# Kernel tuning notes

Hardware: AMD Instinct MI355X
Metric: run time of the kernel (lower is better)

Reference implementation:

```python
import jax, jax.numpy as jnp
import numpy as np

# ---- model dims (match torch para_dict) ----
B, F1, F2, F_OUT = 16, 32, 64, 10
B0, B1, B2 = 32, 16, 8           # bandwidths: input / layer1 / layer2
M1, M2 = 2 * B1 - 1, 2 * B2 - 1  # padded spectral width over signed m
NUM_POINTS = 1
EPS = 1e-5

_LF = np.concatenate([[0.0], np.cumsum(np.log(np.arange(1.0, 200.0)))])  # _LF[i] = log(i!)

def _betas(b):
    return np.pi * (2.0 * np.arange(2 * b) + 1.0) / (4.0 * b)

def _quad_weights(b):
    # Driscoll-Healy quadrature weights on the 2b beta grid
    beta = _betas(b)
    k = np.arange(b)[:, None]
    s = np.sum(np.sin((2 * k + 1) * beta[None, :]) / (2 * k + 1), axis=0)
    return (2.0 / b) * np.sin(beta) * s

def _wig(l, m, n, betas):
    # small Wigner d^l_{m,n}(beta), vectorized over betas (float64)
    kmin, kmax = max(0, m - n), min(l + m, l - n)
    k = np.arange(kmin, kmax + 1)
    pref = 0.5 * (_LF[l + m] + _LF[l - m] + _LF[l + n] + _LF[l - n])
    coef = (-1.0) ** k * np.exp(pref - _LF[k] - _LF[l + m - k] - _LF[l - n - k] - _LF[n - m + k])
    cb, sb = np.cos(betas / 2)[:, None], np.sin(betas / 2)[:, None]
    return (coef * cb ** (2 * l + m - n - 2 * k) * sb ** (n - m + 2 * k)).sum(1)

def _build():
    b0g, b1g, b2g = _betas(B0), _betas(B1), _betas(B2)
    w0, w1q = _quad_weights(B0), _quad_weights(B1)
    d1f = np.zeros((B1, 2 * B0, M1))        # S2 forward: w_j * d^l_{m0}(beta_j)
    d1i = np.zeros((B1, 2 * B1, M1, M1))    # SO3 inverse at layer-1 grid, * (2l+1)
    d2f = np.zeros((B2, 2 * B1, M2, M2))    # SO3 forward at layer-1 grid, * w_j
    d2i = np.zeros((B2, 2 * B2, M2, M2))    # SO3 inverse at layer-2 grid, * (2l+1)
    mask1, mask2 = np.zeros((B1, M1)), np.zeros((B2, M2, M2))
    for l in range(B1):
        o = (B1 - 1) - l
        mask1[l, o:o + 2 * l + 1] = 1.0
        for m in range(-l, l + 1):
            d1f[l, :, o + m + l] = w0 * _wig(l, m, 0, b0g)
            for n in range(-l, l + 1):
                d1i[l, :, o + m + l, o + n + l] = (2 * l + 1) * _wig(l, m, n, b1g)
    for l in range(B2):
        o = (B2 - 1) - l
        mask2[l, o:o + 2 * l + 1, o:o + 2 * l + 1] = 1.0
        for m in range(-l, l + 1):
            for n in range(-l, l + 1):
                d2f[l, :, o + m + l, o + n + l] = w1q * _wig(l, m, n, b1g)
                d2i[l, :, o + m + l, o + n + l] = (2 * l + 1) * _wig(l, m, n, b2g)
    return d1f, d1i, d2f, d2i, mask1, mask2

_d1f, _d1i, _d2f, _d2i, _m1, _m2 = _build()
D1F = jnp.asarray(_d1f, jnp.float32)
D1I = jnp.asarray(_d1i, jnp.float32)
D2F = jnp.asarray(_d2f, jnp.float32)
D2I = jnp.asarray(_d2i, jnp.float32)
MASK1 = jnp.asarray(_m1, jnp.float32)
MASK2 = jnp.asarray(_m2, jnp.float32)
IDX1 = jnp.asarray(np.arange(-(B1 - 1), B1) % (2 * B0), jnp.int32)
IDXG1 = jnp.asarray(np.arange(-(B1 - 1), B1) % (2 * B1), jnp.int32)
IDX2 = jnp.asarray(np.arange(-(B2 - 1), B2) % (2 * B1), jnp.int32)
IDXG2 = jnp.asarray(np.arange(-(B2 - 1), B2) % (2 * B2), jnp.int32)

def _so3_ifft(yh, d_inv, idx, n):
    # yh: [B,F,L,M,M] SO3 spectrum -> signal [B,F,2b,2b,2b] on (beta, alpha, gamma)
    f = jnp.einsum('ljmn,bflmn->bfjmn', d_inv, yh)
    z = jnp.zeros(f.shape[:3] + (n, n), dtype=f.dtype)
    z = z.at[..., idx[:, None], idx[None, :]].set(f)
    return jnp.real(jnp.fft.ifft2(z, axes=(-2, -1))) * (n * n)

def _forward(x, w1r, w1i, w2r, w2i, conv3_w, conv3_b, bn_gamma, bn_beta, fc_w, fc_b):
    # ---- S2 convolution (b_in=B0 -> b_out=B1) ----
    xm = jnp.take(jnp.fft.fft(x, axis=-1), IDX1, axis=-1)      # alpha FFT, signed m  [B,1,2B0,M1]
    xh = jnp.einsum('ljm,bcjm->bclm', D1F, xm)                 # S2 FFT  [B,1,B1,M1]
    w1 = (w1r + 1j * w1i) * MASK1                              # [1,F1,B1,M1]
    yh1 = jnp.einsum('bclm,cfln->bflmn', xh, jnp.conj(w1))     # outer product -> SO3 spectrum
    r1 = jax.nn.relu(_so3_ifft(yh1, D1I, IDXG1, 2 * B1))       # [B,F1,2B1,2B1,2B1]
    # ---- SO3 convolution (b_in=B1 -> b_out=B2) ----
    xf2 = jnp.fft.fft2(r1, axes=(-2, -1))                      # over (alpha, gamma)
    xmn = xf2[..., IDX2[:, None], IDX2[None, :]]               # [B,F1,2B1,M2,M2]
    xh2 = jnp.einsum('ljmn,bcjmn->bclmn', D2F, xmn)            # SO3 FFT [B,F1,B2,M2,M2]
    w2 = (w2r + 1j * w2i) * MASK2                              # [F1,F2,B2,M2,M2]
    yh2 = jnp.einsum('bclmk,cflnk->bflmn', xh2, jnp.conj(w2))  # x_hat @ w_hat^H per l
    r2 = jax.nn.relu(_so3_ifft(yh2, D2I, IDXG2, 2 * B2))       # [B,F2,2B2,2B2,2B2]
    # ---- head: conv1d -> relu -> batchnorm(train) -> linear ----
    feat = r2[:, :, 0, 0, 0].reshape(B, 1, NUM_POINTS * F2)
    c3 = jax.lax.conv_general_dilated(feat, conv3_w, (1,), 'VALID',
                                      dimension_numbers=('NCH', 'OIH', 'NCH'))
    r3 = jax.nn.relu(c3 + conv3_b[None, :, None])              # [B,10,57]
    mu = jnp.mean(r3, axis=(0, 2), keepdims=True)
    var = jnp.mean((r3 - mu) ** 2, axis=(0, 2), keepdims=True)
    bn = bn_gamma[None, :, None] * (r3 - mu) * jax.lax.rsqrt(var + EPS) + bn_beta[None, :, None]
    return bn.reshape(B, -1) @ fc_w.T + fc_b

def setup_inputs():
    key = jax.random.key(0)
    ks = jax.random.split(key, 8)
    f = jnp.float32
    return {
        "x": jax.random.normal(ks[0], (B, 1, 2 * B0, 2 * B0), f),
        "w1r": 0.1 * jax.random.normal(ks[1], (1, F1, B1, M1), f),
        "w1i": 0.1 * jax.random.normal(ks[2], (1, F1, B1, M1), f),
        "w2r": 0.05 * jax.random.normal(ks[3], (F1, F2, B2, M2, M2), f),
        "w2i": 0.05 * jax.random.normal(ks[4], (F1, F2, B2, M2, M2), f),
        "conv3_w": 0.3 * jax.random.normal(ks[5], (10, 1, 8), f),
        "conv3_b": jnp.zeros((10,), f),
        "bn_gamma": jnp.ones((10,), f),
        "bn_beta": jnp.zeros((10,), f),
        "fc_w": 0.05 * jax.random.normal(ks[6], (F_OUT, 10 * (NUM_POINTS * F2 - 8 + 1)), f),
        "fc_b": jnp.zeros((F_OUT,), f),
    }

def reference(x, w1r, w1i, w2r, w2i, conv3_w, conv3_b, bn_gamma, bn_beta, fc_w, fc_b):
    return _forward(x, w1r, w1i, w2r, w2i, conv3_w, conv3_b, bn_gamma, bn_beta, fc_w, fc_b)
```

## Files before the change

kernel.cpp:

```cpp
#include <hip/hip_runtime.h>
#include <math.h>

#ifndef M_PI
#define M_PI 3.14159265358979323846
#endif

#define OFF_TRIG 708
#define OFF_D1F 900
#define OFF_D1I 32644
#define OFF_D2F 540548
#define OFF_S2  598148
#define OFF_XH  599948
#define OFF_XMN 615820
#define OFF_U   7988620
#define OFF_FEAT 9831820
#define OFF_SENT 9832844

typedef float v2f __attribute__((ext_vector_type(2)));
typedef float v4f __attribute__((ext_vector_type(4)));

static __device__ __forceinline__ int iabs_(int v) { return v < 0 ? -v : v; }

static __device__ __forceinline__ v2f mkv2(float a, float b) {
    v2f r; r.x = a; r.y = b; return r;
}
static __device__ __forceinline__ v2f ldv2(float2 a) { return mkv2(a.x, a.y); }

static __device__ __forceinline__ double powi_d(double x, int e) {
    double r = 1.0;
    while (e) { if (e & 1) r *= x; x *= x; e >>= 1; }
    return r;
}

__global__ __launch_bounds__(256) void k0a_tables(float* __restrict__ ws) {
    int t = threadIdx.x;
    for (int i = t; i < 1024; i += 256) ws[OFF_FEAT + i] = 0.f;
    const unsigned* wsu = (const unsigned*)ws;
    if (wsu[OFF_SENT] == 0x1CEB00DAu && wsu[OFF_SENT + 1] == 0x0DDBA11u) return;

    double* T = (double*)ws;
    __shared__ double lg[64];
    if (t < 64) lg[t] = (t == 0) ? 0.0 : log((double)t);
    __syncthreads();
    if (t == 0) {
        double s = 0.0;
        for (int i = 0; i < 64; ++i) { s += lg[i]; T[i] = s; }
    }
    if (t < 64) {
        double beta = M_PI * (2.0 * t + 1.0) / 128.0;
        double s = 0.0;
        for (int k = 0; k < 32; ++k) s += sin((2.0 * k + 1.0) * beta) / (2.0 * k + 1.0);
        T[64 + t] = 2.0 / 32.0 * sin(beta) * s;
        T[160 + t] = cos(0.5 * beta);
        T[224 + t] = sin(0.5 * beta);
    }
    if (t >= 64 && t < 96) {
        int j = t - 64;
        double beta = M_PI * (2.0 * j + 1.0) / 64.0;
        double s = 0.0;
        for (int k = 0; k < 16; ++k) s += sin((2.0 * k + 1.0) * beta) / (2.0 * k + 1.0);
        T[128 + j] = 2.0 / 16.0 * sin(beta) * s;
        T[288 + j] = cos(0.5 * beta);
        T[320 + j] = sin(0.5 * beta);
    }
    if (t == 96) {
        T[352] = cos(M_PI / 64.0);
        T[353] = sin(M_PI / 64.0);
    }
    float2* F = (float2*)(ws + OFF_TRIG);
    if (t < 32) {
        double a = 2.0 * M_PI * (double)t / 32.0;
        F[t] = make_float2((float)cos(a), (float)sin(a));
    }
    if (t >= 128 && t < 192) {
        int i = t - 128;
        double a = 2.0 * M_PI * (double)i / 64.0;
        F[32 + i] = make_float2((float)cos(a), (float)sin(a));
    }
}

__device__ double wig_fast(int l, int m, int n, double cb, double sb, const double* LF) {
    int kmin = max(0, m - n), kmax = min(l + m, l - n);
    if (kmax < kmin) return 0.0;
    double lc = 0.5 * (LF[l + m] + LF[l - m] + LF[l + n] + LF[l - n])
              - LF[kmin] - LF[l + m - kmin] - LF[l - n - kmin] - LF[n - m + kmin];
    double t = exp(lc) * powi_d(cb, 2 * l + m - n - 2 * kmin)
                       * powi_d(sb, n - m + 2 * kmin);
    if (kmin & 1) t = -t;
    double ratio = (sb * sb) / (cb * cb);
    double s = t;
    for (int k = kmin; k < kmax; ++k) {
        t *= -(((double)(l + m - k) * (double)(l - n - k)) /
               ((double)(k + 1) * (double)(n - m + k + 1))) * ratio;
        s += t;
    }
    return s;
}

__global__ __launch_bounds__(256) void k0_consts(float* __restrict__ ws) {
    const unsigned* wsu = (const unsigned*)ws;
    if (wsu[OFF_SENT] == 0x1CEB00DAu && wsu[OFF_SENT + 1] == 0x0DDBA11u) return;

    const double* T = (const double*)ws;
    __shared__ double LF[64];
    int tid = threadIdx.x;
    if (tid < 64) LF[tid] = T[tid];
    __syncthreads();
    int gid = blockIdx.x * 256 + tid;
    if (gid >= 599048) return;

    if (gid < 31744) {
        int mh = gid % 31, j = (gid / 31) % 64, l = gid / (31 * 64);
        int m = mh - 15;
        double v = 0.0;
        if (iabs_(m) <= l)
            v = T[64 + j] * wig_fast(l, m, 0, T[160 + j], T[224 + j], LF);
        ws[OFF_D1F + gid] = (float)v;
    } else if (gid < 539648) {
        int r = gid - 31744;
        int nh = r & 31;
        int l  = (r >> 5) & 15;
        int mh = (r >> 9) % 31;
        int j  = r / (512 * 31);
        int m = mh - 15, n = nh - 15;
        double v = 0.0;
        if (nh < 31 && iabs_(m) <= l && iabs_(n) <= l)
            v = (2.0 * l + 1.0) * wig_fast(l, m, n, T[288 + j], T[320 + j], LF);
        ws[OFF_D1I + r] = (float)v;
    } else if (gid < 597248) {
        int r = gid - 539648;
        int l = r & 7;
        int pq = (r >> 3) % 225;
        int j = r / 1800;
        int mh = pq / 15, nh = pq % 15;
        int m = mh - 7, n = nh - 7;
        double v = 0.0;
        if (iabs_(m) <= l && iabs_(n) <= l)
            v = T[128 + j] * wig_fast(l, m, n, T[288 + j], T[320 + j], LF);
        ws[OFF_D2F + r] = (float)v;
    } else {
        int r = gid - 597248;
        int nh = r % 15, mh = (r / 15) % 15, l = r / 225;
        int m = mh - 7, n = nh - 7;
        double v = 0.0;
        if (iabs_(m) <= l && iabs_(n) <= l)
            v = (2.0 * l + 1.0) * wig_fast(l, m, n, T[352], T[353], LF);
        ws[OFF_S2 + r] = (float)v;
    }
}

__global__ __launch_bounds__(256) void k1_xh(const float* __restrict__ x,
                                             float* __restrict__ ws,
                                             float2* __restrict__ xh) {
    __shared__ float  xs[64 * 64];
    __shared__ float2 xm[64 * 8];
    __shared__ float2 cs64[64];
    int c = blockIdx.x, b = blockIdx.y, tid = threadIdx.x;
    if (c == 0 && b == 0 && tid == 0) {
        unsigned* wsu = (unsigned*)ws;
        wsu[OFF_SENT] = 0x1CEB00DAu;
        wsu[OFF_SENT + 1] = 0x0DDBA11u;
    }
    int mh0 = c * 8;
    int cnt = min(8, 31 - mh0);
    for (int i = tid; i < 4096; i += 256) xs[i] = x[b * 4096 + i];
    if (tid < 64) cs64[tid] = ((const float2*)(ws + OFF_TRIG))[32 + tid];
    __syncthreads();
    for (int i = tid; i < 512; i += 256) {
        int j = i >> 3, mi = i & 7;
        if (mi < cnt) {
            int mu = mh0 + mi - 15;
            float re = 0.f, im = 0.f;
            for (int t = 0; t < 64; ++t) {
                float2 w = cs64[(mu * t) & 63];
                float xv = xs[j * 64 + t];
                re += xv * w.x;
                im -= xv * w.y;
            }
            xm[i] = make_float2(re, im);
        }
    }
    __syncthreads();
    const float* D1F = ws + OFF_D1F;
    if (tid < 128) {
        int l = tid >> 3, mi = tid & 7;
        if (mi < cnt) {
            int mh = mh0 + mi;
            float re = 0.f, im = 0.f;
            for (int j = 0; j < 64; ++j) {
                float d = D1F[(l * 64 + j) * 31 + mh];
                float2 v = xm[j * 8 + mi];
                re += d * v.x;
                im += d * v.y;
            }
            xh[b * 496 + l * 31 + mh] = make_float2(re, im);
        }
    }
}

__global__ __launch_bounds__(256) void k2_planes(const float* __restrict__ w1r,
                                                 const float* __restrict__ w1i,
                                                 const float* __restrict__ ws,
                                                 float2* __restrict__ xmn) {
    __shared__ char ar[13568];
    __shared__ float2 cs2[32];
    float2* As  = (float2*)ar;
    float2* Wv  = (float2*)(ar + 4096);
    float2* fH  = (float2*)(ar + 8192);
    float2* FC  = (float2*)ar;
    float2* tls = (float2*)(ar + 4672);
    float*  ssb = (float*)(ar + 9296);
    float2* gg  = (float2*)ar;
    float2* Cc  = (float2*)(ar + 4864);

    int j = blockIdx.x, f = blockIdx.y, b = blockIdx.z;
    int tid = threadIdx.x;
    const float2* xh = (const float2*)(ws + OFF_XH);

    if (tid < 32) cs2[tid] = ((const float2*)(ws + OFF_TRIG))[tid];
    for (int i = tid; i < 496; i += 256) As[i] = xh[b * 496 + i];
    for (int i = tid; i < 512; i += 256) {
        int l = i >> 5, nh = i & 31;
        bool val = (nh < 31 && iabs_(nh - 15) <= l);
        int nhc = val ? nh : 15;
        int base = f * 496 + l * 31;
        float wr1 = w1r[base + nhc], wi1 = w1i[base + nhc];
        float wr2 = w1r[base + 30 - nhc], wi2 = w1i[base + 30 - nhc];
        float s = (nh & 1) ? 1.f : -1.f;
        float vr = 0.5f * (wr1 + s * wr2);
        float vi = 0.5f * (-wi1 + s * wi2);
        Wv[i] = val ? make_float2(vr, vi) : make_float2(0.f, 0.f);
    }
    __syncthreads();
    if (tid < 128) {
        int mm = tid >> 3;
        int nh0 = (tid & 7) * 4;
        int mrow = mm + 15;
        v2f a0 = {0.f, 0.f}, a1 = {0.f, 0.f}, a2 = {0.f, 0.f}, a3 = {0.f, 0.f};
        const float* Dbase = ws + OFF_D1I + ((j * 31 + mrow) * 16) * 32 + nh0;
        for (int l = mm; l < 16; ++l) {
            float2 a = As[l * 31 + mrow];
            v4f w01 = *(const v4f*)(Wv + l * 32 + nh0);
            v4f w23 = *(const v4f*)(Wv + l * 32 + nh0 + 2);
            v4f d = *(const v4f*)(Dbase + l * 32);
            v2f w, p;
            w = w01.xy; p = a.x * w + a.y * mkv2(-w.y, w.x); a0 += d.x * p;
            w = w01.zw; p = a.x * w + a.y * mkv2(-w.y, w.x); a1 += d.y * p;
            w = w23.xy; p = a.x * w + a.y * mkv2(-w.y, w.x); a2 += d.z * p;
            w = w23.zw; p = a.x * w + a.y * mkv2(-w.y, w.x); a3 += d.w * p;
        }
        float2* fr = fH + mm * 34 + nh0;
        fr[0] = make_float2(a0.x, a0.y);
        fr[1] = make_float2(a1.x, a1.y);
        fr[2] = make_float2(a2.x, a2.y);
        fr[3] = make_float2(a3.x, a3.y);
    }
    __syncthreads();
    if (tid < 128) {
        int mm = tid >> 3, n0 = tid & 7;
        const float2* frow = fH + mm * 34 + n0;
        v2f f0 = ldv2(frow[0]), g1 = ldv2(frow[8]), g2 = ldv2(frow[16]), g3 = ldv2(frow[24]);
        v2f E = f0 + g2, F = f0 - g2, G = g1 + g3, H = g1 - g3;
        int base = mm * 9 + n0;
        FC[0 * 146 + base] = make_float2(E.x + G.x, E.y + G.y);
        FC[1 * 146 + base] = make_float2(F.x - H.y, F.y + H.x);
        FC[2 * 146 + base] = make_float2(E.x - G.x, E.y - G.y);
        FC[3 * 146 + base] = make_float2(F.x + H.y, F.y - H.x);
    }
    __syncthreads();
    if (tid < 128) {
        int mm = tid >> 3, v0 = tid & 7;
        const float2* fc = FC + (v0 & 3) * 146 + mm * 9;
        v2f S0 = {0.f,0.f}, S1 = {0.f,0.f}, S2 = {0.f,0.f}, S3 = {0.f,0.f};
        v2f w = ldv2(cs2[(17 * v0) & 31]);
        v2f st = ldv2(cs2[v0]);
        {
            v2f fv;
            fv = ldv2(fc[0]); S1 += fv.x * w + fv.y * mkv2(-w.y, w.x);
            w = w.x * st + w.y * mkv2(-st.y, st.x);
            fv = ldv2(fc[1]); S2 += fv.x * w + fv.y * mkv2(-w.y, w.x);
            w = w.x * st + w.y * mkv2(-st.y, st.x);
            fv = ldv2(fc[2]); S3 += fv.x * w + fv.y * mkv2(-w.y, w.x);
            w = w.x * st + w.y * mkv2(-st.y, st.x);
            fv = ldv2(fc[3]); S0 += fv.x * w + fv.y * mkv2(-w.y, w.x);
            w = w.x * st + w.y * mkv2(-st.y, st.x);
            fv = ldv2(fc[4]); S1 += fv.x * w + fv.y * mkv2(-w.y, w.x);
            w = w.x * st + w.y * mkv2(-st.y, st.x);
            fv = ldv2(fc[5]); S2 += fv.x * w + fv.y * mkv2(-w.y, w.x);
            w = w.x * st + w.y * mkv2(-st.y, st.x);
            fv = ldv2(fc[6]); S3 += fv.x * w + fv.y * mkv2(-w.y, w.x);
            w = w.x * st + w.y * mkv2(-st.y, st.x);
            fv = ldv2(fc[7]); S0 += fv.x * w + fv.y * mkv2(-w.y, w.x);
        }
        v2f E = S0 + S2, F = S0 - S2, G = S1 + S3, H = S1 - S3;
        v2f A0 = E + G, A2 = E - G;
        v2f iH = mkv2(-H.y, H.x);
        v2f A1 = F + iH, A3 = F - iH;
        float2* trow = tls + mm * 34;
        trow[v0]      = make_float2(A0.x, A0.y);
        trow[v0 + 8]  = make_float2(A1.x, A1.y);
        trow[v0 + 16] = make_float2(A2.x, A2.y);
        trow[v0 + 24] = make_float2(A3.x, A3.y);
    } else if (tid < 162) {
        tls[16 * 34 + (tid - 128)] = make_float2(0.f, 0.f);
    }
    __syncthreads();
    {
        int v = tid & 31, u0 = tid >> 5;
        v2f Z0 = {0.f,0.f}, Z1 = {0.f,0.f}, Z2 = {0.f,0.f}, Z3 = {0.f,0.f};
        v2f y1 = ldv2(cs2[u0]);
        v2f y2 = ldv2(cs2[(2 * u0) & 31]);
        v2f y3 = ldv2(cs2[(3 * u0) & 31]);
        v2f y4 = ldv2(cs2[(4 * u0) & 31]);
        v2f st = y4;
#pragma unroll
        for (int mb = 1; mb <= 13; mb += 4) {
            float2 tv;
            tv = tls[mb * 34 + v];
            Z1 += tv.x * y1; Z1 += tv.y * mkv2(-y1.y, y1.x);
            tv = tls[(mb + 1) * 34 + v];
            Z2 += tv.x * y2; Z2 += tv.y * mkv2(-y2.y, y2.x);
            tv = tls[(mb + 2) * 34 + v];
            Z3 += tv.x * y3; Z3 += tv.y * mkv2(-y3.y, y3.x);
            tv = tls[(mb + 3) * 34 + v];
            Z0 += tv.x * y4; Z0 += tv.y * mkv2(-y4.y, y4.x);
            y1 = y1.x * st + y1.y * mkv2(-st.y, st.x);
            y2 = y2.x * st + y2.y * mkv2(-st.y, st.x);
            y3 = y3.x * st + y3.y * mkv2(-st.y, st.x);
            y4 = y4.x * st + y4.y * mkv2(-st.y, st.x);
        }
        float E = Z0.x + Z2.x, F = Z0.x - Z2.x;
        float G = Z1.x + Z3.x;
        float Hy = Z1.y - Z3.y;
        float s0 = E + G, s2 = E - G;
        float s1 = F - Hy, s3 = F + Hy;
        float t0x = tls[v].x;
        ssb[u0 * 33 + v]        = fmaxf(t0x + 2.f * s0, 0.f);
        ssb[(u0 + 8) * 33 + v]  = fmaxf(t0x + 2.f * s1, 0.f);
        ssb[(u0 + 16) * 33 + v] = fmaxf(t0x + 2.f * s2, 0.f);
        ssb[(u0 + 24) * 33 + v] = fmaxf(t0x + 2.f * s3, 0.f);
    }
    __syncthreads();
    {
        int u = tid >> 3, q = tid & 7;
        int qm = q & 3;
        float r1 = (qm == 0) ? 1.f : (qm == 2 ? -1.f : 0.f);
        float r2 = (qm & 1) ? -1.f : 1.f;
        float i1 = (qm == 1) ? -1.f : (qm == 3 ? 1.f : 0.f);
        v2f g = {0.f, 0.f};
        const float* srow = ssb + u * 33;
        v2f w = mkv2(1.f, 0.f);
        v2f st = ldv2(cs2[(-q) & 31]);
#pragma unroll
        for (int vb = 0; vb < 8; ++vb) {
            float s0 = srow[vb], s1 = srow[vb + 8], s2 = srow[vb + 16], s3 = srow[vb + 24];
            float zre = (s0 + r2 * s2) + r1 * (s1 + s3);
            float zim = i1 * (s1 - s3);
            g += zre * w; g += zim * mkv2(-w.y, w.x);
            w = w.x * st + w.y * mkv2(-st.y, st.x);
        }
        gg[u * 18 + 7 + q] = make_float2(g.x, g.y);
        if (q) gg[u * 18 + 7 - q] = make_float2(g.x, -g.y);
    }
    __syncthreads();
    if (tid < 120) {
        int u0 = tid / 15, qh = tid % 15;
        v2f g0 = ldv2(gg[u0 * 18 + qh]);
        v2f g1 = ldv2(gg[(u0 + 8) * 18 + qh]);
        v2f g2 = ldv2(gg[(u0 + 16) * 18 + qh]);
        v2f g3 = ldv2(gg[(u0 + 24) * 18 + qh]);
        v2f E = g0 + g2, F = g0 - g2, G = g1 + g3, H = g1 - g3;
        int base = u0 * 19 + qh;
        Cc[0 * 152 + base] = make_float2(E.x + G.x, E.y + G.y);
        Cc[1 * 152 + base] = make_float2(F.x + H.y, F.y - H.x);
        Cc[2 * 152 + base] = make_float2(E.x - G.x, E.y - G.y);
        Cc[3 * 152 + base] = make_float2(F.x - H.y, F.y + H.x);
    }
    __syncthreads();
    if (tid < 113) {
        int ph, qh;
        if (tid < 105) { ph = 8 + tid / 15; qh = tid % 15; }
        else           { ph = 7; qh = 7 + (tid - 105); }
        int p = ph - 7;
        const float2* cp = Cc + (p & 3) * 152 + qh;
        v2f h = {0.f, 0.f};
        v2f w = mkv2(1.f, 0.f);
        v2f st = ldv2(cs2[(-p) & 31]);
#pragma unroll
        for (int u0 = 0; u0 < 8; ++u0) {
            v2f gv = ldv2(cp[u0 * 19]);
            h += gv.x * w + gv.y * mkv2(-w.y, w.x);
            w = w.x * st + w.y * mkv2(-st.y, st.x);
        }
        float2* outp = xmn + ((size_t)((b * 32 + f) * 32 + j)) * 225;
        outp[ph * 15 + qh] = make_float2(h.x, h.y);
        if (ph > 7 || qh > 7)
            outp[(14 - ph) * 15 + (14 - qh)] = make_float2(h.x, -h.y);
    }
}

__global__ __launch_bounds__(256) void k34_U(const float* __restrict__ ws,
                                             const float2* __restrict__ xmn,
                                             float2* __restrict__ U) {
    __shared__ float2 xh2s[1800];
    __shared__ float  S2s[1800];
    int bc = blockIdx.x, tid = threadIdx.x;

    for (int i = tid; i < 1800; i += 256) S2s[i] = ws[OFF_S2 + i];

    v2f a0 = {0.f,0.f}, a1 = {0.f,0.f}, a2 = {0.f,0.f}, a3 = {0.f,0.f};
    v2f a4 = {0.f,0.f}, a5 = {0.f,0.f}, a6 = {0.f,0.f}, a7 = {0.f,0.f};
    if (tid < 225) {
        const float2* xp = xmn + (size_t)bc * 7200;
        const v4f* dw = (const v4f*)(ws + OFF_D2F);
        for (int j = 0; j < 32; ++j) {
            float2 xvf = xp[j * 225 + tid];
            v2f xv = mkv2(xvf.x, xvf.y);
            v4f dA = dw[(j * 225 + tid) * 2];
            v4f dB = dw[(j * 225 + tid) * 2 + 1];
            a0 += dA.x * xv; a1 += dA.y * xv; a2 += dA.z * xv; a3 += dA.w * xv;
            a4 += dB.x * xv; a5 += dB.y * xv; a6 += dB.z * xv; a7 += dB.w * xv;
        }
        xh2s[0 * 225 + tid] = make_float2(a0.x, a0.y);
        xh2s[1 * 225 + tid] = make_float2(a1.x, a1.y);
        xh2s[2 * 225 + tid] = make_float2(a2.x, a2.y);
        xh2s[3 * 225 + tid] = make_float2(a3.x, a3.y);
        xh2s[4 * 225 + tid] = make_float2(a4.x, a4.y);
        xh2s[5 * 225 + tid] = make_float2(a5.x, a5.y);
        xh2s[6 * 225 + tid] = make_float2(a6.x, a6.y);
        xh2s[7 * 225 + tid] = make_float2(a7.x, a7.y);
    }
    __syncthreads();

    for (int idx = tid; idx < 1800; idx += 256) {
        int l = idx / 225;
        int rem = idx - l * 225;
        int n = rem / 15, k = rem - n * 15;
        v2f a = {0.f, 0.f};
        for (int m = 0; m < 15; ++m) {
            float s = S2s[(l * 15 + m) * 15 + n];
            float2 vf = xh2s[l * 225 + m * 15 + k];
            a += s * mkv2(vf.x, vf.y);
        }
        U[(size_t)bc * 1800 + idx] = make_float2(a.x, a.y);
    }
}

__global__ __launch_bounds__(256) void k5_feat(const float* __restrict__ w2r,
                                               const float* __restrict__ w2i,
                                               const float2* __restrict__ U,
                                               float* __restrict__ feat) {
    __shared__ char ar[57856];
    float2* Us  = (float2*)ar;
    float2* Wsh = (float2*)(ar + 28928);
    int bx = blockIdx.x;
    int c = bx >> 5, l = (bx >> 2) & 7, fc = bx & 3;
    int tid = threadIdx.x;

    for (int i = tid; i < 3600; i += 256) {
        int b = i / 225, t = i - b * 225;
        Us[b * 226 + t] = U[(size_t)(b * 32 + c) * 1800 + l * 225 + t];
    }
    for (int i = tid; i < 3600; i += 256) {
        int fr = i / 225;
        int f = fc * 16 + fr;
        int t = i - fr * 225;
        int n = t / 15, k = t - n * 15;
        bool valid = (iabs_(n - 7) <= l) && (iabs_(k - 7) <= l);
        int wi = ((c * 64 + f) * 8 + l) * 225 + t;
        Wsh[fr * 226 + t] = valid ? make_float2(w2r[wi], w2i[wi]) : make_float2(0.f, 0.f);
    }
    if (tid < 16) {
        Us[tid * 226 + 225]  = make_float2(0.f, 0.f);
        Wsh[tid * 226 + 225] = make_float2(0.f, 0.f);
    }
    __syncthreads();
    int b = tid >> 4, fl = tid & 15;
    const v4f* up = (const v4f*)(Us + b * 226);
    const v4f* wp = (const v4f*)(Wsh + fl * 226);
    v2f acc2 = {0.f, 0.f};
    for (int t = 0; t < 113; ++t) {
        v4f u4 = up[t], w4 = wp[t];
        acc2 += u4.xy * w4.xy;
        acc2 += u4.zw * w4.zw;
    }
    float accv = acc2.x + acc2.y;
    atomicAdd(&feat[b * 64 + fc * 16 + fl], accv);
}

__global__ __launch_bounds__(640) void k6_head(const float* __restrict__ feat,
                                               const float* __restrict__ w3,
                                               const float* __restrict__ b3,
                                               const float* __restrict__ gamma,
                                               const float* __restrict__ beta,
                                               const float* __restrict__ fcw,
                                               const float* __restrict__ fcb,
                                               float* __restrict__ out) {
    __shared__ float fL[1024];
    __shared__ float w3L[80];
    __shared__ float b3L[10];
    __shared__ float r3[9120];
    __shared__ float scaleL[10], shiftL[10];
    int tid = threadIdx.x;
    for (int i = tid; i < 1024; i += 640) fL[i] = fmaxf(feat[i], 0.f);
    if (tid < 80) w3L[tid] = w3[tid];
    if (tid >= 80 && tid < 90) b3L[tid - 80] = b3[tid - 80];
    __syncthreads();
    for (int i = tid; i < 9120; i += 640) {
        int ch = i / 912;
        int r = i % 912;
        int b = r / 57, pos = r % 57;
        float acc = b3L[ch];
#pragma unroll
        for (int t = 0; t < 8; ++t) acc += fL[b * 64 + pos + t] * w3L[ch * 8 + t];
        r3[ch * 912 + r] = fmaxf(acc, 0.0f);
    }
    __syncthreads();
    int wave = tid >> 6, lane = tid & 63;
    if (wave < 10) {
        float s = 0.f, s2 = 0.f;
        for (int i = lane; i < 912; i += 64) {
            float v = r3[wave * 912 + i];
            s += v;
            s2 += v * v;
        }
        for (int off = 32; off > 0; off >>= 1) {
            s += __shfl_down(s, off);
            s2 += __shfl_down(s2, off);
        }
        if (lane == 0) {
            float mu = s / 912.0f;
            float var = s2 / 912.0f - mu * mu;
            float sc = gamma[wave] * rsqrtf(var + 1e-5f);
            scaleL[wave] = sc;
            shiftL[wave] = beta[wave] - mu * sc;
        }
    }
    __syncthreads();
    {
        int pair = tid >> 2, sub = tid & 3;
        int b = pair / 10, o = pair % 10;
        float acc = 0.f;
        for (int idx = sub; idx < 570; idx += 4) {
            int ch = idx / 57, pos = idx - ch * 57;
            acc += (r3[ch * 912 + b * 57 + pos] * scaleL[ch] + shiftL[ch])
                   * fcw[o * 570 + idx];
        }
        acc += __shfl_down(acc, 2);
        acc += __shfl_down(acc, 1);
        if (sub == 0) out[b * 10 + o] = acc + fcb[o];
    }
}

extern "C" void kernel_launch(void* const* d_in, const int* in_sizes, int n_in,
                              void* d_out, int out_size, void* d_ws, size_t ws_size,
                              hipStream_t stream) {
    const float* x   = (const float*)d_in[0];
    const float* w1r = (const float*)d_in[1];
    const float* w1i = (const float*)d_in[2];
    const float* w2r = (const float*)d_in[3];
    const float* w2i = (const float*)d_in[4];
    const float* c3w = (const float*)d_in[5];
    const float* c3b = (const float*)d_in[6];
    const float* bng = (const float*)d_in[7];
    const float* bnb = (const float*)d_in[8];
    const float* fcw = (const float*)d_in[9];
    const float* fcb = (const float*)d_in[10];
    float* ws = (float*)d_ws;
    float* out = (float*)d_out;

    hipLaunchKernelGGL(k0a_tables, dim3(1), dim3(256), 0, stream, ws);
    hipLaunchKernelGGL(k0_consts, dim3(2341), dim3(256), 0, stream, ws);
    hipLaunchKernelGGL(k1_xh, dim3(4, 16), dim3(256), 0, stream, x, ws,
                       (float2*)(ws + OFF_XH));
    hipLaunchKernelGGL(k2_planes, dim3(32, 32, 16), dim3(256), 0, stream, w1r, w1i, ws,
                       (float2*)(ws + OFF_XMN));
    hipLaunchKernelGGL(k34_U, dim3(512), dim3(256), 0, stream, ws,
                       (const float2*)(ws + OFF_XMN), (float2*)(ws + OFF_U));
    hipLaunchKernelGGL(k5_feat, dim3(1024), dim3(256), 0, stream, w2r, w2i,
                       (const float2*)(ws + OFF_U), ws + OFF_FEAT);
    hipLaunchKernelGGL(k6_head, dim3(1), dim3(640), 0, stream, ws + OFF_FEAT,
                       c3w, c3b, bng, bnb, fcw, fcb, out);
}
```

Measured before the change: 271.8 us.

## Fuse plane synthesis with SO3 forward transform into one per-(f,b) kernel

```diff
diff --git a/kernel.cpp b/kernel.cpp
--- a/kernel.cpp
+++ b/kernel.cpp
@@ -11,7 +11,6 @@
 #define OFF_D2F 540548
 #define OFF_S2  598148
 #define OFF_XH  599948
-#define OFF_XMN 615820
 #define OFF_U   7988620
 #define OFF_FEAT 9831820
 #define OFF_SENT 9832844
@@ -198,28 +197,30 @@
     }
 }
 
-__global__ __launch_bounds__(256) void k2_planes(const float* __restrict__ w1r,
-                                                 const float* __restrict__ w1i,
-                                                 const float* __restrict__ ws,
-                                                 float2* __restrict__ xmn) {
-    __shared__ char ar[13568];
+__global__ __launch_bounds__(512) void k2f(const float* __restrict__ w1r,
+                                           const float* __restrict__ w1i,
+                                           const float* __restrict__ ws,
+                                           float2* __restrict__ U) {
+    __shared__ char ar[21600];
     __shared__ float2 cs2[32];
-    float2* As  = (float2*)ar;
-    float2* Wv  = (float2*)(ar + 4096);
-    float2* fH  = (float2*)(ar + 8192);
-    float2* FC  = (float2*)ar;
-    float2* tls = (float2*)(ar + 4672);
-    float*  ssb = (float*)(ar + 9296);
-    float2* gg  = (float2*)ar;
-    float2* Cc  = (float2*)(ar + 4864);
-
-    int j = blockIdx.x, f = blockIdx.y, b = blockIdx.z;
+    __shared__ float2 Wv[512];
+
+    int f = blockIdx.x, b = blockIdx.y;
     int tid = threadIdx.x;
-    const float2* xh = (const float2*)(ws + OFF_XH);
+    int half = tid >> 8;
+    int t = tid & 255;
+    char* arena = ar + half * 9728;
+    float2* fH  = (float2*)arena;
+    float2* FC  = (float2*)(arena + 4624);
+    float2* tls = (float2*)arena;
+    float*  ssb = (float*)(arena + 4864);
+    float2* gg  = (float2*)arena;
+    float2* Cc  = (float2*)(arena + 4864);
+    float2* hs  = (float2*)arena;
 
     if (tid < 32) cs2[tid] = ((const float2*)(ws + OFF_TRIG))[tid];
-    for (int i = tid; i < 496; i += 256) As[i] = xh[b * 496 + i];
-    for (int i = tid; i < 512; i += 256) {
+    {
+        int i = tid;
         int l = i >> 5, nh = i & 31;
         bool val = (nh < 31 && iabs_(nh - 15) <= l);
         int nhc = val ? nh : 15;
@@ -227,222 +228,224 @@
         float wr1 = w1r[base + nhc], wi1 = w1i[base + nhc];
         float wr2 = w1r[base + 30 - nhc], wi2 = w1i[base + 30 - nhc];
         float s = (nh & 1) ? 1.f : -1.f;
-        float vr = 0.5f * (wr1 + s * wr2);
-        float vi = 0.5f * (-wi1 + s * wi2);
-        Wv[i] = val ? make_float2(vr, vi) : make_float2(0.f, 0.f);
-    }
-    __syncthreads();
-    if (tid < 128) {
-        int mm = tid >> 3;
-        int nh0 = (tid & 7) * 4;
-        int mrow = mm + 15;
-        v2f a0 = {0.f, 0.f}, a1 = {0.f, 0.f}, a2 = {0.f, 0.f}, a3 = {0.f, 0.f};
-        const float* Dbase = ws + OFF_D1I + ((j * 31 + mrow) * 16) * 32 + nh0;
-        for (int l = mm; l < 16; ++l) {
-            float2 a = As[l * 31 + mrow];
-            v4f w01 = *(const v4f*)(Wv + l * 32 + nh0);
-            v4f w23 = *(const v4f*)(Wv + l * 32 + nh0 + 2);
-            v4f d = *(const v4f*)(Dbase + l * 32);
-            v2f w, p;
-            w = w01.xy; p = a.x * w + a.y * mkv2(-w.y, w.x); a0 += d.x * p;
-            w = w01.zw; p = a.x * w + a.y * mkv2(-w.y, w.x); a1 += d.y * p;
-            w = w23.xy; p = a.x * w + a.y * mkv2(-w.y, w.x); a2 += d.z * p;
-            w = w23.zw; p = a.x * w + a.y * mkv2(-w.y, w.x); a3 += d.w * p;
-        }
-        float2* fr = fH + mm * 34 + nh0;
-        fr[0] = make_float2(a0.x, a0.y);
-        fr[1] = make_float2(a1.x, a1.y);
-        fr[2] = make_float2(a2.x, a2.y);
-        fr[3] = make_float2(a3.x, a3.y);
-    }
-    __syncthreads();
-    if (tid < 128) {
-        int mm = tid >> 3, n0 = tid & 7;
-        const float2* frow = fH + mm * 34 + n0;
-        v2f f0 = ldv2(frow[0]), g1 = ldv2(frow[8]), g2 = ldv2(frow[16]), g3 = ldv2(frow[24]);
-        v2f E = f0 + g2, F = f0 - g2, G = g1 + g3, H = g1 - g3;
-        int base = mm * 9 + n0;
-        FC[0 * 146 + base] = make_float2(E.x + G.x, E.y + G.y);
-        FC[1 * 146 + base] = make_float2(F.x - H.y, F.y + H.x);
-        FC[2 * 146 + base] = make_float2(E.x - G.x, E.y - G.y);
-        FC[3 * 146 + base] = make_float2(F.x + H.y, F.y - H.x);
-    }
-    __syncthreads();
-    if (tid < 128) {
-        int mm = tid >> 3, v0 = tid & 7;
-        const float2* fc = FC + (v0 & 3) * 146 + mm * 9;
-        v2f S0 = {0.f,0.f}, S1 = {0.f,0.f}, S2 = {0.f,0.f}, S3 = {0.f,0.f};
-        v2f w = ldv2(cs2[(17 * v0) & 31]);
-        v2f st = ldv2(cs2[v0]);
+        Wv[i] = val ? make_float2(0.5f * (wr1 + s * wr2), 0.5f * (-wi1 + s * wi2))
+                    : make_float2(0.f, 0.f);
+    }
+    int mm = t >> 3, nh0 = (t & 7) * 4, mrow = mm + 15;
+    v2f areg[16];
+    if (t < 128) {
+        const float2* xhp = (const float2*)(ws + OFF_XH) + b * 496;
+#pragma unroll
+        for (int l = 0; l < 16; ++l) {
+            float2 av = xhp[l * 31 + mrow];
+            areg[l] = mkv2(av.x, av.y);
+        }
+    }
+    __syncthreads();
+    int v0 = t & 7;
+    v2f w3i = ldv2(cs2[(17 * v0) & 31]);
+    v2f st3 = ldv2(cs2[v0]);
+    int v4 = t & 31, u04 = t >> 5;
+    v2f y1i = ldv2(cs2[u04 & 31]);
+    v2f y2i = ldv2(cs2[(2 * u04) & 31]);
+    v2f y3i = ldv2(cs2[(3 * u04) & 31]);
+    v2f y4i = ldv2(cs2[(4 * u04) & 31]);
+    int u5 = t >> 3, q5 = t & 7, qm5 = q5 & 3;
+    float r1 = (qm5 == 0) ? 1.f : (qm5 == 2 ? -1.f : 0.f);
+    float r2 = (qm5 & 1) ? -1.f : 1.f;
+    float i1 = (qm5 == 1) ? -1.f : (qm5 == 3 ? 1.f : 0.f);
+    v2f st5 = ldv2(cs2[(32 - q5) & 31]);
+    int u06 = t / 15, qh6 = t % 15;
+    int ph7, qh7;
+    if (t < 105) { ph7 = 8 + t / 15; qh7 = t % 15; }
+    else         { ph7 = 7; qh7 = 7 + (t - 105); }
+    int p7 = ph7 - 7;
+    v2f st7 = ldv2(cs2[(32 - p7) & 31]);
+    int lh8 = tid / 225, pq8 = tid - lh8 * 225;
+    const v4f* dw = (const v4f*)(ws + OFF_D2F);
+    float2* hs0 = (float2*)ar;
+    float2* hs1 = (float2*)(ar + 9728);
+    v2f ac0 = {0.f,0.f}, ac1 = {0.f,0.f}, ac2 = {0.f,0.f}, ac3 = {0.f,0.f};
+
+    for (int jt = 0; jt < 16; ++jt) {
+        int j = 2 * jt + half;
+        if (t < 128) {
+            v2f a0 = {0.f,0.f}, a1 = {0.f,0.f}, a2 = {0.f,0.f}, a3 = {0.f,0.f};
+            const float* Dbase = ws + OFF_D1I + ((j * 31 + mrow) * 16) * 32 + nh0;
+#pragma unroll
+            for (int l = 0; l < 16; ++l) {
+                if (l >= mm) {
+                    v2f a = areg[l];
+                    v2f ap = mkv2(-a.y, a.x);
+                    v4f w01 = *(const v4f*)(Wv + l * 32 + nh0);
+                    v4f w23 = *(const v4f*)(Wv + l * 32 + nh0 + 2);
+                    v4f d = *(const v4f*)(Dbase + l * 32);
+                    v2f p;
+                    p = w01.x * a + w01.y * ap; a0 += d.x * p;
+                    p = w01.z * a + w01.w * ap; a1 += d.y * p;
+                    p = w23.x * a + w23.y * ap; a2 += d.z * p;
+                    p = w23.z * a + w23.w * ap; a3 += d.w * p;
+                }
+            }
+            float2* fr = fH + mm * 34 + nh0;
+            fr[0] = make_float2(a0.x, a0.y);
+            fr[1] = make_float2(a1.x, a1.y);
+            fr[2] = make_float2(a2.x, a2.y);
+            fr[3] = make_float2(a3.x, a3.y);
+            {
+                int n0 = t & 7;
+                const float2* frow = fH + mm * 34 + n0;
+                v2f f0 = ldv2(frow[0]), g1 = ldv2(frow[8]);
+                v2f g2 = ldv2(frow[16]), g3 = ldv2(frow[24]);
+                v2f E = f0 + g2, F = f0 - g2, G = g1 + g3, H = g1 - g3;
+                int basei = mm * 9 + n0;
+                FC[0 * 146 + basei] = make_float2(E.x + G.x, E.y + G.y);
+                FC[1 * 146 + basei] = make_float2(F.x - H.y, F.y + H.x);
+                FC[2 * 146 + basei] = make_float2(E.x - G.x, E.y - G.y);
+                FC[3 * 146 + basei] = make_float2(F.x + H.y, F.y - H.x);
+            }
+            {
+                const float2* fc = FC + (v0 & 3) * 146 + mm * 9;
+                v2f S0 = {0.f,0.f}, S1 = {0.f,0.f}, S2 = {0.f,0.f}, S3 = {0.f,0.f};
+                v2f w = w3i, st = st3, fv;
+                fv = ldv2(fc[0]); S1 += fv.x * w + fv.y * mkv2(-w.y, w.x);
+                w = w.x * st + w.y * mkv2(-st.y, st.x);
+                fv = ldv2(fc[1]); S2 += fv.x * w + fv.y * mkv2(-w.y, w.x);
+                w = w.x * st + w.y * mkv2(-st.y, st.x);
+                fv = ldv2(fc[2]); S3 += fv.x * w + fv.y * mkv2(-w.y, w.x);
+                w = w.x * st + w.y * mkv2(-st.y, st.x);
+                fv = ldv2(fc[3]); S0 += fv.x * w + fv.y * mkv2(-w.y, w.x);
+                w = w.x * st + w.y * mkv2(-st.y, st.x);
+                fv = ldv2(fc[4]); S1 += fv.x * w + fv.y * mkv2(-w.y, w.x);
+                w = w.x * st + w.y * mkv2(-st.y, st.x);
+                fv = ldv2(fc[5]); S2 += fv.x * w + fv.y * mkv2(-w.y, w.x);
+                w = w.x * st + w.y * mkv2(-st.y, st.x);
+                fv = ldv2(fc[6]); S3 += fv.x * w + fv.y * mkv2(-w.y, w.x);
+                w = w.x * st + w.y * mkv2(-st.y, st.x);
+                fv = ldv2(fc[7]); S0 += fv.x * w + fv.y * mkv2(-w.y, w.x);
+                v2f E = S0 + S2, F = S0 - S2, G = S1 + S3, H = S1 - S3;
+                v2f A0 = E + G, A2 = E - G;
+                v2f iH = mkv2(-H.y, H.x);
+                v2f A1 = F + iH, A3 = F - iH;
+                float2* trow = tls + mm * 34;
+                trow[v0]      = make_float2(A0.x, A0.y);
+                trow[v0 + 8]  = make_float2(A1.x, A1.y);
+                trow[v0 + 16] = make_float2(A2.x, A2.y);
+                trow[v0 + 24] = make_float2(A3.x, A3.y);
+            }
+        } else if (t < 162) {
+            tls[16 * 34 + (t - 128)] = make_float2(0.f, 0.f);
+        }
+        __syncthreads();
         {
-            v2f fv;
-            fv = ldv2(fc[0]); S1 += fv.x * w + fv.y * mkv2(-w.y, w.x);
-            w = w.x * st + w.y * mkv2(-st.y, st.x);
-            fv = ldv2(fc[1]); S2 += fv.x * w + fv.y * mkv2(-w.y, w.x);
-            w = w.x * st + w.y * mkv2(-st.y, st.x);
-            fv = ldv2(fc[2]); S3 += fv.x * w + fv.y * mkv2(-w.y, w.x);
-            w = w.x * st + w.y * mkv2(-st.y, st.x);
-            fv = ldv2(fc[3]); S0 += fv.x * w + fv.y * mkv2(-w.y, w.x);
-            w = w.x * st + w.y * mkv2(-st.y, st.x);
-            fv = ldv2(fc[4]); S1 += fv.x * w + fv.y * mkv2(-w.y, w.x);
-            w = w.x * st + w.y * mkv2(-st.y, st.x);
-            fv = ldv2(fc[5]); S2 += fv.x * w + fv.y * mkv2(-w.y, w.x);
-            w = w.x * st + w.y * mkv2(-st.y, st.x);
-            fv = ldv2(fc[6]); S3 += fv.x * w + fv.y * mkv2(-w.y, w.x);
-            w = w.x * st + w.y * mkv2(-st.y, st.x);
-            fv = ldv2(fc[7]); S0 += fv.x * w + fv.y * mkv2(-w.y, w.x);
-        }
-        v2f E = S0 + S2, F = S0 - S2, G = S1 + S3, H = S1 - S3;
-        v2f A0 = E + G, A2 = E - G;
-        v2f iH = mkv2(-H.y, H.x);
-        v2f A1 = F + iH, A3 = F - iH;
-        float2* trow = tls + mm * 34;
-        trow[v0]      = make_float2(A0.x, A0.y);
-        trow[v0 + 8]  = make_float2(A1.x, A1.y);
-        trow[v0 + 16] = make_float2(A2.x, A2.y);
-        trow[v0 + 24] = make_float2(A3.x, A3.y);
-    } else if (tid < 162) {
-        tls[16 * 34 + (tid - 128)] = make_float2(0.f, 0.f);
-    }
-    __syncthreads();
-    {
-        int v = tid & 31, u0 = tid >> 5;
-        v2f Z0 = {0.f,0.f}, Z1 = {0.f,0.f}, Z2 = {0.f,0.f}, Z3 = {0.f,0.f};
-        v2f y1 = ldv2(cs2[u0]);
-        v2f y2 = ldv2(cs2[(2 * u0) & 31]);
-        v2f y3 = ldv2(cs2[(3 * u0) & 31]);
-        v2f y4 = ldv2(cs2[(4 * u0) & 31]);
-        v2f st = y4;
+            v2f Z0 = {0.f,0.f}, Z1 = {0.f,0.f}, Z2 = {0.f,0.f}, Z3 = {0.f,0.f};
+            v2f y1 = y1i, y2 = y2i, y3 = y3i, y4 = y4i, st = y4i;
 #pragma unroll
-        for (int mb = 1; mb <= 13; mb += 4) {
-            float2 tv;
-            tv = tls[mb * 34 + v];
-            Z1 += tv.x * y1; Z1 += tv.y * mkv2(-y1.y, y1.x);
-            tv = tls[(mb + 1) * 34 + v];
-            Z2 += tv.x * y2; Z2 += tv.y * mkv2(-y2.y, y2.x);
-            tv = tls[(mb + 2) * 34 + v];
-            Z3 += tv.x * y3; Z3 += tv.y * mkv2(-y3.y, y3.x);
-            tv = tls[(mb + 3) * 34 + v];
-            Z0 += tv.x * y4; Z0 += tv.y * mkv2(-y4.y, y4.x);
-            y1 = y1.x * st + y1.y * mkv2(-st.y, st.x);
-            y2 = y2.x * st + y2.y * mkv2(-st.y, st.x);
-            y3 = y3.x * st + y3.y * mkv2(-st.y, st.x);
-            y4 = y4.x * st + y4.y * mkv2(-st.y, st.x);
-        }
-        float E = Z0.x + Z2.x, F = Z0.x - Z2.x;
-        float G = Z1.x + Z3.x;
-        float Hy = Z1.y - Z3.y;
-        float s0 = E + G, s2 = E - G;
-        float s1 = F - Hy, s3 = F + Hy;
-        float t0x = tls[v].x;
-        ssb[u0 * 33 + v]        = fmaxf(t0x + 2.f * s0, 0.f);
-        ssb[(u0 + 8) * 33 + v]  = fmaxf(t0x + 2.f * s1, 0.f);
-        ssb[(u0 + 16) * 33 + v] = fmaxf(t0x + 2.f * s2, 0.f);
-        ssb[(u0 + 24) * 33 + v] = fmaxf(t0x + 2.f * s3, 0.f);
-    }
-    __syncthreads();
-    {
-        int u = tid >> 3, q = tid & 7;
-        int qm = q & 3;
-        float r1 = (qm == 0) ? 1.f : (qm == 2 ? -1.f : 0.f);
-        float r2 = (qm & 1) ? -1.f : 1.f;
-        float i1 = (qm == 1) ? -1.f : (qm == 3 ? 1.f : 0.f);
-        v2f g = {0.f, 0.f};
-        const float* srow = ssb + u * 33;
-        v2f w = mkv2(1.f, 0.f);
-        v2f st = ldv2(cs2[(-q) & 31]);
+            for (int mb = 1; mb <= 13; mb += 4) {
+                float2 tv;
+                tv = tls[mb * 34 + v4];
+                Z1 += tv.x * y1; Z1 += tv.y * mkv2(-y1.y, y1.x);
+                tv = tls[(mb + 1) * 34 + v4];
+                Z2 += tv.x * y2; Z2 += tv.y * mkv2(-y2.y, y2.x);
+                tv = tls[(mb + 2) * 34 + v4];
+                Z3 += tv.x * y3; Z3 += tv.y * mkv2(-y3.y, y3.x);
+                tv = tls[(mb + 3) * 34 + v4];
+                Z0 += tv.x * y4; Z0 += tv.y * mkv2(-y4.y, y4.x);
+                y1 = y1.x * st + y1.y * mkv2(-st.y, st.x);
+                y2 = y2.x * st + y2.y * mkv2(-st.y, st.x);
+                y3 = y3.x * st + y3.y * mkv2(-st.y, st.x);
+                y4 = y4.x * st + y4.y * mkv2(-st.y, st.x);
+            }
+            float E = Z0.x + Z2.x, F = Z0.x - Z2.x;
+            float G = Z1.x + Z3.x;
+            float Hy = Z1.y - Z3.y;
+            float s0 = E + G, s2 = E - G;
+            float s1 = F - Hy, s3 = F + Hy;
+            float t0x = tls[v4].x;
+            ssb[u04 * 33 + v4]        = fmaxf(t0x + 2.f * s0, 0.f);
+            ssb[(u04 + 8) * 33 + v4]  = fmaxf(t0x + 2.f * s1, 0.f);
+            ssb[(u04 + 16) * 33 + v4] = fmaxf(t0x + 2.f * s2, 0.f);
+            ssb[(u04 + 24) * 33 + v4] = fmaxf(t0x + 2.f * s3, 0.f);
+        }
+        __syncthreads();
+        {
+            v2f g = {0.f, 0.f};
+            const float* srow = ssb + u5 * 33;
+            v2f w = mkv2(1.f, 0.f), st = st5;
 #pragma unroll
-        for (int vb = 0; vb < 8; ++vb) {
-            float s0 = srow[vb], s1 = srow[vb + 8], s2 = srow[vb + 16], s3 = srow[vb + 24];
-            float zre = (s0 + r2 * s2) + r1 * (s1 + s3);
-            float zim = i1 * (s1 - s3);
-            g += zre * w; g += zim * mkv2(-w.y, w.x);
-            w = w.x * st + w.y * mkv2(-st.y, st.x);
-        }
-        gg[u * 18 + 7 + q] = make_float2(g.x, g.y);
-        if (q) gg[u * 18 + 7 - q] = make_float2(g.x, -g.y);
-    }
-    __syncthreads();
-    if (tid < 120) {
-        int u0 = tid / 15, qh = tid % 15;
-        v2f g0 = ldv2(gg[u0 * 18 + qh]);
-        v2f g1 = ldv2(gg[(u0 + 8) * 18 + qh]);
-        v2f g2 = ldv2(gg[(u0 + 16) * 18 + qh]);
-        v2f g3 = ldv2(gg[(u0 + 24) * 18 + qh]);
-        v2f E = g0 + g2, F = g0 - g2, G = g1 + g3, H = g1 - g3;
-        int base = u0 * 19 + qh;
-        Cc[0 * 152 + base] = make_float2(E.x + G.x, E.y + G.y);
-        Cc[1 * 152 + base] = make_float2(F.x + H.y, F.y - H.x);
-        Cc[2 * 152 + base] = make_float2(E.x - G.x, E.y - G.y);
-        Cc[3 * 152 + base] = make_float2(F.x - H.y, F.y + H.x);
-    }
-    __syncthreads();
-    if (tid < 113) {
-        int ph, qh;
-        if (tid < 105) { ph = 8 + tid / 15; qh = tid % 15; }
-        else           { ph = 7; qh = 7 + (tid - 105); }
-        int p = ph - 7;
-        const float2* cp = Cc + (p & 3) * 152 + qh;
-        v2f h = {0.f, 0.f};
-        v2f w = mkv2(1.f, 0.f);
-        v2f st = ldv2(cs2[(-p) & 31]);
+            for (int vb = 0; vb < 8; ++vb) {
+                float s0 = srow[vb], s1 = srow[vb + 8];
+                float s2 = srow[vb + 16], s3 = srow[vb + 24];
+                float zre = (s0 + r2 * s2) + r1 * (s1 + s3);
+                float zim = i1 * (s1 - s3);
+                g += zre * w; g += zim * mkv2(-w.y, w.x);
+                w = w.x * st + w.y * mkv2(-st.y, st.x);
+            }
+            gg[u5 * 18 + 7 + q5] = make_float2(g.x, g.y);
+            if (q5) gg[u5 * 18 + 7 - q5] = make_float2(g.x, -g.y);
+        }
+        __syncthreads();
+        if (t < 120) {
+            v2f g0 = ldv2(gg[u06 * 18 + qh6]);
+            v2f g1 = ldv2(gg[(u06 + 8) * 18 + qh6]);
+            v2f g2 = ldv2(gg[(u06 + 16) * 18 + qh6]);
+            v2f g3 = ldv2(gg[(u06 + 24) * 18 + qh6]);
+            v2f E = g0 + g2, F = g0 - g2, G = g1 + g3, H = g1 - g3;
+            int basei = u06 * 19 + qh6;
+            Cc[0 * 152 + basei] = make_float2(E.x + G.x, E.y + G.y);
+            Cc[1 * 152 + basei] = make_float2(F.x + H.y, F.y - H.x);
+            Cc[2 * 152 + basei] = make_float2(E.x - G.x, E.y - G.y);
+            Cc[3 * 152 + basei] = make_float2(F.x - H.y, F.y + H.x);
+        }
+        __syncthreads();
+        if (t < 113) {
+            const float2* cp = Cc + (p7 & 3) * 152 + qh7;
+            v2f h = {0.f, 0.f};
+            v2f w = mkv2(1.f, 0.f), st = st7;
 #pragma unroll
-        for (int u0 = 0; u0 < 8; ++u0) {
-            v2f gv = ldv2(cp[u0 * 19]);
-            h += gv.x * w + gv.y * mkv2(-w.y, w.x);
-            w = w.x * st + w.y * mkv2(-st.y, st.x);
-        }
-        float2* outp = xmn + ((size_t)((b * 32 + f) * 32 + j)) * 225;
-        outp[ph * 15 + qh] = make_float2(h.x, h.y);
-        if (ph > 7 || qh > 7)
-            outp[(14 - ph) * 15 + (14 - qh)] = make_float2(h.x, -h.y);
-    }
-}
-
-__global__ __launch_bounds__(256) void k34_U(const float* __restrict__ ws,
-                                             const float2* __restrict__ xmn,
-                                             float2* __restrict__ U) {
-    __shared__ float2 xh2s[1800];
-    __shared__ float  S2s[1800];
-    int bc = blockIdx.x, tid = threadIdx.x;
-
-    for (int i = tid; i < 1800; i += 256) S2s[i] = ws[OFF_S2 + i];
-
-    v2f a0 = {0.f,0.f}, a1 = {0.f,0.f}, a2 = {0.f,0.f}, a3 = {0.f,0.f};
-    v2f a4 = {0.f,0.f}, a5 = {0.f,0.f}, a6 = {0.f,0.f}, a7 = {0.f,0.f};
-    if (tid < 225) {
-        const float2* xp = xmn + (size_t)bc * 7200;
-        const v4f* dw = (const v4f*)(ws + OFF_D2F);
-        for (int j = 0; j < 32; ++j) {
-            float2 xvf = xp[j * 225 + tid];
-            v2f xv = mkv2(xvf.x, xvf.y);
-            v4f dA = dw[(j * 225 + tid) * 2];
-            v4f dB = dw[(j * 225 + tid) * 2 + 1];
-            a0 += dA.x * xv; a1 += dA.y * xv; a2 += dA.z * xv; a3 += dA.w * xv;
-            a4 += dB.x * xv; a5 += dB.y * xv; a6 += dB.z * xv; a7 += dB.w * xv;
-        }
-        xh2s[0 * 225 + tid] = make_float2(a0.x, a0.y);
-        xh2s[1 * 225 + tid] = make_float2(a1.x, a1.y);
-        xh2s[2 * 225 + tid] = make_float2(a2.x, a2.y);
-        xh2s[3 * 225 + tid] = make_float2(a3.x, a3.y);
-        xh2s[4 * 225 + tid] = make_float2(a4.x, a4.y);
-        xh2s[5 * 225 + tid] = make_float2(a5.x, a5.y);
-        xh2s[6 * 225 + tid] = make_float2(a6.x, a6.y);
-        xh2s[7 * 225 + tid] = make_float2(a7.x, a7.y);
-    }
-    __syncthreads();
-
-    for (int idx = tid; idx < 1800; idx += 256) {
+            for (int u0 = 0; u0 < 8; ++u0) {
+                v2f gv = ldv2(cp[u0 * 19]);
+                h += gv.x * w + gv.y * mkv2(-w.y, w.x);
+                w = w.x * st + w.y * mkv2(-st.y, st.x);
+            }
+            hs[ph7 * 15 + qh7] = make_float2(h.x, h.y);
+            if (ph7 > 7 || qh7 > 7)
+                hs[(14 - ph7) * 15 + (14 - qh7)] = make_float2(h.x, -h.y);
+        }
+        __syncthreads();
+        if (tid < 450) {
+            v2f h0 = ldv2(hs0[pq8]);
+            v2f h1 = ldv2(hs1[pq8]);
+            v4f d0 = dw[(2 * jt) * 450 + pq8 * 2 + lh8];
+            v4f d1 = dw[(2 * jt + 1) * 450 + pq8 * 2 + lh8];
+            ac0 += d0.x * h0 + d1.x * h1;
+            ac1 += d0.y * h0 + d1.y * h1;
+            ac2 += d0.z * h0 + d1.z * h1;
+            ac3 += d0.w * h0 + d1.w * h1;
+        }
+        __syncthreads();
+    }
+    float2* xh2L = (float2*)ar;
+    float*  S2f  = (float*)(ar + 14400);
+    if (tid < 450) {
+        xh2L[(lh8 * 4 + 0) * 225 + pq8] = make_float2(ac0.x, ac0.y);
+        xh2L[(lh8 * 4 + 1) * 225 + pq8] = make_float2(ac1.x, ac1.y);
+        xh2L[(lh8 * 4 + 2) * 225 + pq8] = make_float2(ac2.x, ac2.y);
+        xh2L[(lh8 * 4 + 3) * 225 + pq8] = make_float2(ac3.x, ac3.y);
+    }
+    for (int i = tid; i < 1800; i += 512) S2f[i] = ws[OFF_S2 + i];
+    __syncthreads();
+    for (int idx = tid; idx < 1800; idx += 512) {
         int l = idx / 225;
         int rem = idx - l * 225;
         int n = rem / 15, k = rem - n * 15;
         v2f a = {0.f, 0.f};
         for (int m = 0; m < 15; ++m) {
-            float s = S2s[(l * 15 + m) * 15 + n];
-            float2 vf = xh2s[l * 225 + m * 15 + k];
+            float s = S2f[(l * 15 + m) * 15 + n];
+            float2 vf = xh2L[l * 225 + m * 15 + k];
             a += s * mkv2(vf.x, vf.y);
         }
-        U[(size_t)bc * 1800 + idx] = make_float2(a.x, a.y);
+        U[(size_t)(b * 32 + f) * 1800 + idx] = make_float2(a.x, a.y);
     }
 }
 
@@ -573,10 +576,8 @@
     hipLaunchKernelGGL(k0_consts, dim3(2341), dim3(256), 0, stream, ws);
     hipLaunchKernelGGL(k1_xh, dim3(4, 16), dim3(256), 0, stream, x, ws,
                        (float2*)(ws + OFF_XH));
-    hipLaunchKernelGGL(k2_planes, dim3(32, 32, 16), dim3(256), 0, stream, w1r, w1i, ws,
-                       (float2*)(ws + OFF_XMN));
-    hipLaunchKernelGGL(k34_U, dim3(512), dim3(256), 0, stream, ws,
-                       (const float2*)(ws + OFF_XMN), (float2*)(ws + OFF_U));
+    hipLaunchKernelGGL(k2f, dim3(32, 16), dim3(512), 0, stream, w1r, w1i, ws,
+                       (float2*)(ws + OFF_U));
     hipLaunchKernelGGL(k5_feat, dim3(1024), dim3(256), 0, stream, w2r, w2i,
                        (const float2*)(ws + OFF_U), ws + OFF_FEAT);
     hipLaunchKernelGGL(k6_head, dim3(1), dim3(640), 0, stream, ws + OFF_FEAT,
```

Measured after the change: 414.4 us. 1.52x slower.
